# Performance work log

Measured on AMD Instinct MI355X. Metric: run time of the kernel, lower is better.

Reference implementation:

```python
import jax, jax.numpy as jnp
import numpy as np

MUL = 32            # multiplicity of each irrep (0e and 1o)
N_NODES = 50000
N_EDGES = 800000
NUM_NEIGHBORS = 16.0
SQRT3 = 3.0 ** 0.5
SILU_NORM = 1.6790  # e3nn normalize2mom constant for silu: 1/sqrt(E[silu(z)^2]), z~N(0,1)


def split_irreps(x):
    # x: [..., 128] laid out as 32x0e (32) ++ 32x1o (32*3)
    x0 = x[..., :MUL]
    x1 = x[..., MUL:].reshape(x.shape[:-1] + (MUL, 3))
    return x0, x1


def merge_irreps(x0, x1):
    return jnp.concatenate([x0, x1.reshape(x1.shape[:-2] + (MUL * 3,))], axis=-1)


def fctp_scalar(x0, x1, a, W0, W1, fan_in):
    # FullyConnectedTensorProduct(in_irreps, '1x0e', out_irreps): per-irrep linear
    # mixing scaled by scalar attr; e3nn path weight sqrt(dim_out/fan_in) times the
    # orthonormal CG (1/sqrt(dim)) folds to 1/sqrt(fan_in) for every irrep.
    s = a / jnp.sqrt(jnp.asarray(fan_in, x0.dtype))
    o0 = (x0 @ W0) * s
    o1 = jnp.einsum('nud,uw->nwd', x1, W1) * s[..., None]
    return o0, o1


def setup_inputs() -> dict:
    key = jax.random.key(0)
    ks = jax.random.split(key, 17)
    inp = dict(
        node_input=jax.random.normal(ks[0], (N_NODES, 4 * MUL), jnp.float32),
        node_attr=jnp.ones((N_NODES, 1), jnp.float32),
        edge_src=jax.random.randint(ks[1], (N_EDGES,), 0, N_NODES),
        edge_dst=jax.random.randint(ks[2], (N_EDGES,), 0, N_NODES),
        edge_attr=jax.random.normal(ks[3], (N_EDGES, 4), jnp.float32),
        edge_scalars=jax.random.normal(ks[4], (N_EDGES, 64), jnp.float32),
    )
    p = lambda k, sh: jax.random.normal(k, sh, jnp.float32)  # e3nn init: N(0,1)
    inp.update(
        W_sc0=p(ks[5], (MUL, MUL)), W_sc1=p(ks[6], (MUL, MUL)),
        W_l1_0=p(ks[7], (MUL, MUL)), W_l1_1=p(ks[8], (MUL, MUL)),
        W_fc1=p(ks[9], (64, 64)), W_fc2=p(ks[10], (64, 4 * MUL)),
        W_l2_A0=p(ks[11], (MUL, MUL)), W_l2_B0=p(ks[12], (MUL, MUL)),
        W_l2_C1=p(ks[13], (MUL, MUL)), W_l2_D1=p(ks[14], (MUL, MUL)),
        W_l3_A=p(ks[15], (MUL, 1)), W_l3_B=p(ks[16], (MUL, 1)),
    )
    return inp


def reference(node_input, node_attr, edge_src, edge_dst, edge_attr, edge_scalars,
              W_sc0, W_sc1, W_l1_0, W_l1_1, W_fc1, W_fc2,
              W_l2_A0, W_l2_B0, W_l2_C1, W_l2_D1, W_l3_A, W_l3_B):
    n = node_input.shape[0]
    x0, x1 = split_irreps(node_input)

    # per-edge TP weights from MLP on edge scalars (e3nn FullyConnectedNet)
    h = SILU_NORM * jax.nn.silu(edge_scalars @ (W_fc1 / 8.0))  # /sqrt(64)
    weight = h @ (W_fc2 / 8.0)                                  # [E, 128]

    # self connection (sc) and lin1 (FCTP with scalar node attr, fan_in = 32)
    sc0, sc1 = fctp_scalar(x0, x1, node_attr, W_sc0, W_sc1, MUL)
    f0, f1 = fctp_scalar(x0, x1, node_attr, W_l1_0, W_l1_1, MUL)

    # gather source-node features per edge
    g0 = f0[edge_src]          # [E, 32]
    g1 = f1[edge_src]          # [E, 32, 3]
    e0 = edge_attr[:, :1]      # [E, 1]  0e
    e1 = edge_attr[:, 1:]      # [E, 3]  1o

    # weight layout follows instruction order: (0e*0e->0e), (0e*1o->1o), (1o*0e->1o), (1o*1o->0e)
    wA, wC, wD, wB = (weight[:, :MUL], weight[:, MUL:2 * MUL],
                      weight[:, 2 * MUL:3 * MUL], weight[:, 3 * MUL:])
    # weighted CG tensor product ('uvu'); e3nn path weights sqrt(dim_out) folded with
    # orthonormal wigner-3j entries (1/sqrt(3) for l=1 couplings)
    outA = wA * g0 * e0                                    # [E,32]   0e x 0e -> 0e
    outB = wB * jnp.einsum('euk,ek->eu', g1, e1) / SQRT3   # [E,32]   1o x 1o -> 0e
    outC = (wC * g0)[..., None] * e1[:, None, :]           # [E,32,3] 0e x 1o -> 1o
    outD = wD[..., None] * g1 * e0[..., None]              # [E,32,3] 1o x 0e -> 1o

    # scatter-add aggregation to destination nodes
    seg = lambda v: jax.ops.segment_sum(v, edge_dst, num_segments=n)
    inv = 1.0 / jnp.sqrt(jnp.asarray(NUM_NEIGHBORS, node_input.dtype))
    mA, mB, mC, mD = seg(outA) * inv, seg(outB) * inv, seg(outC) * inv, seg(outD) * inv

    # lin2: irreps_mid (32x0e+32x0e+32x1o+32x1o) -> output, fan_in = 64 per output irrep
    s = node_attr / 8.0  # attr / sqrt(64)
    c0 = (mA @ W_l2_A0 + mB @ W_l2_B0) * s
    c1 = (jnp.einsum('nud,uw->nwd', mC, W_l2_C1)
          + jnp.einsum('nud,uw->nwd', mD, W_l2_D1)) * s[..., None]

    # lin3: irreps_mid -> 0e gate angle (only 0e chunks contribute)
    angle = 0.1 * (mA @ W_l3_A + mB @ W_l3_B) * s          # [N, 1]
    cos, sin = jnp.cos(angle), jnp.sin(angle)              # sc.output_mask is all ones

    return cos * merge_irreps(sc0, sc1) + sin * merge_irreps(c0, c1)
```

## Files before the change

kernel.cpp:

```cpp
#include <hip/hip_runtime.h>
#include <stdint.h>

#define N_NODES 50000
#define N_EDGES 800000
#define CAP 64
#define NTILES 50000
#define NSB 49

typedef _Float16 f16x8 __attribute__((ext_vector_type(8)));
typedef _Float16 f16x2 __attribute__((ext_vector_type(2)));
typedef float    f32x4 __attribute__((ext_vector_type(4)));

static __device__ __forceinline__ uint32_t pk16(float a, float b) {
    return __builtin_bit_cast(uint32_t, __builtin_amdgcn_cvt_pkrtz(a, b));
}
static __device__ __forceinline__ float lo16(uint32_t v) {
    f16x2 h = __builtin_bit_cast(f16x2, v); return (float)h[0];
}
static __device__ __forceinline__ float hi16(uint32_t v) {
    f16x2 h = __builtin_bit_cast(f16x2, v); return (float)h[1];
}

__global__ __launch_bounds__(256) void k_node_f(
        const float* __restrict__ x, const float* __restrict__ attr,
        const float* __restrict__ W0, const float* __restrict__ W1,
        uint32_t* __restrict__ fh)
{
    const int wv = threadIdx.x >> 6;
    const int t  = threadIdx.x & 63;
    const int node = blockIdx.x*4 + wv;
    if (node >= N_NODES) return;
    __shared__ float xs[4][128];
    xs[wv][t]      = x[(size_t)node*128 + t];
    xs[wv][64 + t] = x[(size_t)node*128 + 64 + t];
    float a = attr[node] * 0.17677669529663689f;
    float s0 = 0.f, s1 = 0.f;
    if (t < 32) {
        #pragma unroll
        for (int v = 0; v < 32; ++v) {
            s0 += xs[wv][v] * W0[v*32 + t];
            s1 += xs[wv][32 + v*3 + 0] * W1[v*32 + t];
        }
    } else {
        int u = t - 32;
        #pragma unroll
        for (int v = 0; v < 32; ++v) {
            s0 += xs[wv][32 + v*3 + 1] * W1[v*32 + u];
            s1 += xs[wv][32 + v*3 + 2] * W1[v*32 + u];
        }
    }
    fh[(size_t)node*64 + t] = pk16(s0*a, s1*a);
}

__global__ void k_ticket(const int* __restrict__ dst, int* __restrict__ cnt,
                         uint8_t* __restrict__ slot8) {
    int e = blockIdx.x*256 + threadIdx.x;
    if (e >= N_EDGES) return;
    int d = dst[e];
    int slot = atomicAdd(&cnt[d], 1);
    slot8[e] = (uint8_t)min(slot, 255);
}

__global__ __launch_bounds__(1024) void k_scan1(const int* __restrict__ cnt,
                                                int* __restrict__ offs,
                                                int* __restrict__ bsum) {
    __shared__ int sh[1024];
    int t = threadIdx.x, i = blockIdx.x*1024 + t;
    int v = (i < N_NODES) ? min(cnt[i], CAP) : 0;
    sh[t] = v; __syncthreads();
    #pragma unroll
    for (int off = 1; off < 1024; off <<= 1) {
        int u = (t >= off) ? sh[t - off] : 0;
        __syncthreads();
        sh[t] += u;
        __syncthreads();
    }
    if (i < N_NODES) offs[i] = sh[t] - v;
    if (t == 1023) bsum[blockIdx.x] = sh[t];
}

__global__ void k_scan2(const int* __restrict__ bsum, int* __restrict__ bbase,
                        int* __restrict__ offs) {
    int t = threadIdx.x;
    int v = (t < NSB) ? bsum[t] : 0;
    int inc = v;
    #pragma unroll
    for (int off = 1; off < 64; off <<= 1) {
        int u = __shfl_up(inc, off);
        if (t >= off) inc += u;
    }
    if (t < NSB) bbase[t] = inc - v;
    if (t == NSB - 1) offs[N_NODES] = inc;
}

__global__ __launch_bounds__(1024) void k_scan3(int* __restrict__ offs,
                                                const int* __restrict__ bbase) {
    int i = blockIdx.x*1024 + threadIdx.x;
    if (i < N_NODES) offs[i] += bbase[blockIdx.x];
}

__global__ void k_scatter(const int* __restrict__ dst, const int* __restrict__ esrc,
                          const float* __restrict__ eattr,
                          const uint8_t* __restrict__ slot8,
                          const int* __restrict__ offs,
                          int2* __restrict__ csr_se, float4* __restrict__ csr_e1) {
    int e = blockIdx.x*256 + threadIdx.x;
    if (e >= N_EDGES) return;
    int slot = slot8[e];
    if (slot >= CAP) return;
    int pos = offs[dst[e]] + slot;
    csr_se[pos] = make_int2(e, esrc[e]);
    float4 ea = *(const float4*)(eattr + (size_t)e*4);
    csr_e1[pos] = make_float4(ea.y, ea.z, ea.w, ea.x);
}

__global__ __launch_bounds__(256) void k_edge_w(
    const float* __restrict__ escal, const float* __restrict__ eattr,
    const float* __restrict__ Wfc1, const float* __restrict__ Wfc2,
    uint32_t* __restrict__ weight)
{
    __shared__ __align__(16) _Float16 lds_h[4][16][72];
    __shared__ __align__(16) uint32_t lds_o[4][16][64];

    const int wv   = threadIdx.x >> 6;
    const int lane = threadIdx.x & 63;
    const int rl   = lane & 15;
    const int g4   = lane >> 4;

    f16x8 w1f[2][4];
    #pragma unroll
    for (int ks = 0; ks < 2; ++ks)
      #pragma unroll
      for (int jt = 0; jt < 4; ++jt)
        #pragma unroll
        for (int i = 0; i < 8; ++i)
          w1f[ks][jt][i] = (_Float16)(Wfc1[(ks*32 + g4*8 + i)*64 + jt*16 + rl] * 0.125f);
    f16x8 w2f[2][8];
    #pragma unroll
    for (int ks = 0; ks < 2; ++ks)
      #pragma unroll
      for (int jt = 0; jt < 8; ++jt)
        #pragma unroll
        for (int i = 0; i < 8; ++i)
          w2f[ks][jt][i] = (_Float16)(Wfc2[(ks*32 + g4*8 + i)*128 + jt*16 + rl] * 0.125f);

    const int w  = blockIdx.x*4 + wv;
    const int t0 = w*8;
    const int t1 = (t0 + 8 < NTILES) ? t0 + 8 : NTILES;

    for (int tt = t0; tt < t1; ++tt) {
        const int eb = tt*16;
        f16x8 af[2];
        #pragma unroll
        for (int ks = 0; ks < 2; ++ks) {
            const float* p = escal + (size_t)(eb + rl)*64 + ks*32 + g4*8;
            float4 lo = *(const float4*)(p);
            float4 hi = *(const float4*)(p + 4);
            af[ks][0]=(_Float16)lo.x; af[ks][1]=(_Float16)lo.y;
            af[ks][2]=(_Float16)lo.z; af[ks][3]=(_Float16)lo.w;
            af[ks][4]=(_Float16)hi.x; af[ks][5]=(_Float16)hi.y;
            af[ks][6]=(_Float16)hi.z; af[ks][7]=(_Float16)hi.w;
        }
        float e0L = eattr[(size_t)(eb + rl)*4];

        f32x4 hacc[4];
        #pragma unroll
        for (int jt = 0; jt < 4; ++jt) {
            f32x4 z = {0.f,0.f,0.f,0.f};
            z = __builtin_amdgcn_mfma_f32_16x16x32_f16(af[0], w1f[0][jt], z, 0,0,0);
            z = __builtin_amdgcn_mfma_f32_16x16x32_f16(af[1], w1f[1][jt], z, 0,0,0);
            hacc[jt] = z;
        }
        #pragma unroll
        for (int jt = 0; jt < 4; ++jt)
          #pragma unroll
          for (int r = 0; r < 4; ++r) {
            float v = hacc[jt][r];
            float s = 1.679f * v / (1.f + __expf(-v));
            lds_h[wv][g4*4 + r][jt*16 + rl] = (_Float16)s;
          }
        f16x8 a2[2];
        #pragma unroll
        for (int ks = 0; ks < 2; ++ks)
            a2[ks] = *reinterpret_cast<const f16x8*>(&lds_h[wv][rl][ks*32 + g4*8]);

        f32x4 z[8];
        #pragma unroll
        for (int jt = 0; jt < 8; ++jt) {
            f32x4 zz = {0.f,0.f,0.f,0.f};
            zz = __builtin_amdgcn_mfma_f32_16x16x32_f16(a2[0], w2f[0][jt], zz, 0,0,0);
            zz = __builtin_amdgcn_mfma_f32_16x16x32_f16(a2[1], w2f[1][jt], zz, 0,0,0);
            z[jt] = zz;
        }

        #pragma unroll
        for (int pg = 0; pg < 2; ++pg)
          #pragma unroll
          for (int r = 0; r < 4; ++r) {
            float e0r = __shfl(e0L, g4*4 + r);
            float loA = z[pg][r]     * (0.25f * e0r);
            float hiC = z[2 + pg][r] * 0.25f;
            float loD = z[4 + pg][r] * (0.25f * e0r);
            float hiB = z[6 + pg][r] * 0.14433756729740643f;
            lds_o[wv][g4*4 + r][pg*16 + rl]      = pk16(loA, hiC);
            lds_o[wv][g4*4 + r][32 + pg*16 + rl] = pk16(loD, hiB);
          }

        uint32_t* wg = weight + (size_t)eb*64;
        const uint32_t* lo32 = &lds_o[wv][0][0];
        #pragma unroll
        for (int pq = 0; pq < 4; ++pq) {
            *(uint4*)(wg + pq*256 + lane*4) = *(const uint4*)(lo32 + pq*256 + lane*4);
        }
    }
}

__global__ __launch_bounds__(256, 6) void k_main(
    const float* __restrict__ x, const float* __restrict__ attr,
    const uint32_t* __restrict__ weight, const int2* __restrict__ csr_se,
    const float4* __restrict__ csr_e1,
    const float* __restrict__ Wsc0, const float* __restrict__ Wsc1,
    const float* __restrict__ WA0,  const float* __restrict__ WB0,
    const float* __restrict__ WC1,  const float* __restrict__ WD1,
    const float* __restrict__ W3A,  const float* __restrict__ W3B,
    const uint32_t* __restrict__ fh, const int* __restrict__ offs,
    float* __restrict__ out)
{
    __shared__ float lds_m[4][256];

    const int wv   = threadIdx.x >> 6;
    const int lane = threadIdx.x & 63;
    const int u    = lane & 31;
    const int half = lane >> 5;
    const int node = blockIdx.x*4 + wv;
    if (node >= N_NODES) return;

    const int o0  = __builtin_amdgcn_readfirstlane(offs[node]);
    const int deg = __builtin_amdgcn_readfirstlane(offs[node + 1]) - o0;

    float mAB = 0.f, mCD0 = 0.f, mCD1 = 0.f, mCD2 = 0.f;

    for (int b = 0; b < deg; b += 16) {
        int nb = min(16, deg - b);
        uint32_t wp[16], ga[16], gbv[16];
        #pragma unroll
        for (int j = 0; j < 16; ++j) if (j < nb) {
            int pos = o0 + b + j;
            int2 se = csr_se[pos];
            wp[j] = weight[(size_t)se.x*64 + lane];
            const uint32_t* fr = fh + (size_t)se.y*64;
            ga[j] = fr[u];
            if (half) gbv[j] = fr[32 + u];
        }
        #pragma unroll
        for (int j = 0; j < 16; ++j) if (j < nb) {
            int pos = o0 + b + j;
            float4 v = csr_e1[pos];
            float e1x = v.x, e1y = v.y, e1z = v.z;
            float lo = lo16(wp[j]), hi = hi16(wp[j]);
            if (half == 0) {
                float g0 = lo16(ga[j]);
                mAB += lo * g0;
                float tc = hi * g0;
                mCD0 += tc*e1x; mCD1 += tc*e1y; mCD2 += tc*e1z;
            } else {
                float gx = hi16(ga[j]);
                float gy = lo16(gbv[j]), gz = hi16(gbv[j]);
                mAB += hi * (gx*e1x + gy*e1y + gz*e1z);
                mCD0 += lo*gx; mCD1 += lo*gy; mCD2 += lo*gz;
            }
        }
    }

    float* M = lds_m[wv];
    if (half == 0) {
        M[u] = mAB;
        M[64  + u*3 + 0] = mCD0; M[64  + u*3 + 1] = mCD1; M[64  + u*3 + 2] = mCD2;
    } else {
        M[32 + u] = mAB;
        M[160 + u*3 + 0] = mCD0; M[160 + u*3 + 1] = mCD1; M[160 + u*3 + 2] = mCD2;
    }

    float a    = attr[node];
    float a8   = a * 0.125f;
    float as32 = a * 0.17677669529663689f;

    const float w3 = (half == 0) ? W3A[u] : W3B[u];
    float tpart = (half == 0) ? M[u] * w3 : M[32 + u] * w3;
    #pragma unroll
    for (int off = 32; off > 0; off >>= 1) tpart += __shfl_xor(tpart, off);
    float angle = 0.1f * tpart * a8;
    float sn, cs; __sincosf(angle, &sn, &cs);

    const float* xr = x + (size_t)node*128;
    #pragma unroll
    for (int pass = 0; pass < 2; ++pass) {
        int c = lane + pass*64;
        bool A = (c < 32);
        int cc = c - 32;
        int wq = cc / 3, d = cc - 3*wq;
        int sT = A ? 1 : 3;
        const float* pT1 = A ? &M[0]        : &M[64 + d];
        const float* pT2 = A ? &M[32]       : &M[160 + d];
        const float* pX  = A ? xr           : xr + 32 + d;
        int k = A ? c : wq;
        const float* pWa = (A ? WA0  : WC1)  + k;
        const float* pWb = (A ? WB0  : WD1)  + k;
        const float* pWx = (A ? Wsc0 : Wsc1) + k;
        float s1 = 0.f, s2 = 0.f;
        #pragma unroll
        for (int uu = 0; uu < 32; ++uu) {
            s1 += pT1[uu*sT] * pWa[uu*32] + pT2[uu*sT] * pWb[uu*32];
            s2 += pX[uu*sT]  * pWx[uu*32];
        }
        out[(size_t)node*128 + c] = cs*(s2*as32) + sn*(s1*a8);
    }
}

extern "C" void kernel_launch(void* const* d_in, const int* in_sizes, int n_in,
                              void* d_out, int out_size, void* d_ws, size_t ws_size,
                              hipStream_t stream) {
    const float* node_input = (const float*)d_in[0];
    const float* node_attr  = (const float*)d_in[1];
    const int*   edge_src   = (const int*)  d_in[2];
    const int*   edge_dst   = (const int*)  d_in[3];
    const float* edge_attr  = (const float*)d_in[4];
    const float* edge_scal  = (const float*)d_in[5];
    const float* W_sc0 = (const float*)d_in[6];
    const float* W_sc1 = (const float*)d_in[7];
    const float* W_l10 = (const float*)d_in[8];
    const float* W_l11 = (const float*)d_in[9];
    const float* W_fc1 = (const float*)d_in[10];
    const float* W_fc2 = (const float*)d_in[11];
    const float* W_A0  = (const float*)d_in[12];
    const float* W_B0  = (const float*)d_in[13];
    const float* W_C1  = (const float*)d_in[14];
    const float* W_D1  = (const float*)d_in[15];
    const float* W_3A  = (const float*)d_in[16];
    const float* W_3B  = (const float*)d_in[17];
    float* out = (float*)d_out;

    char* p = (char*)d_ws;
    auto alloc = [&](size_t bytes) { char* r = p; p += (bytes + 15) & ~(size_t)15; return r; };
    uint32_t* fh      = (uint32_t*)alloc((size_t)N_NODES*64*4);
    int*      cnt     = (int*)     alloc((size_t)N_NODES*4);
    int*      offs    = (int*)     alloc((size_t)(N_NODES+1)*4);
    uint8_t*  slot8   = (uint8_t*) alloc((size_t)N_EDGES);
    int*      bsum    = (int*)     alloc((size_t)NSB*4);
    int*      bbase   = (int*)     alloc((size_t)NSB*4);
    int2*     csr_se  = (int2*)    alloc((size_t)N_EDGES*8);
    float4*   csr_e1  = (float4*)  alloc((size_t)N_EDGES*16);
    uint32_t* weight  = (uint32_t*)alloc((size_t)N_EDGES*64*4);

    hipMemsetAsync(cnt, 0, (size_t)N_NODES*4, stream);
    k_node_f <<<(N_NODES+3)/4, 256, 0, stream>>>(node_input, node_attr, W_l10, W_l11, fh);
    k_ticket <<<(N_EDGES+255)/256, 256, 0, stream>>>(edge_dst, cnt, slot8);
    k_scan1  <<<NSB, 1024, 0, stream>>>(cnt, offs, bsum);
    k_scan2  <<<1, 64, 0, stream>>>(bsum, bbase, offs);
    k_scan3  <<<NSB, 1024, 0, stream>>>(offs, bbase);
    k_scatter<<<(N_EDGES+255)/256, 256, 0, stream>>>(edge_dst, edge_src, edge_attr,
               slot8, offs, csr_se, csr_e1);
    k_edge_w <<<1563, 256, 0, stream>>>(edge_scal, edge_attr, W_fc1, W_fc2, weight);
    k_main   <<<(N_NODES+3)/4, 256, 0, stream>>>(node_input, node_attr, weight, csr_se, csr_e1,
               W_sc0, W_sc1, W_A0, W_B0, W_C1, W_D1, W_3A, W_3B, fh, offs, out);
}
```

Before: 389.2 us.

## Move self-connection linear into node kernel and share weight loads across node pairs

Computes the self-connection (sc) linear in k_node_f and stores it as packed fp16 per node, so k_main no longer reads x or applies Wsc. The epilogue of k_main now has each thread handle one output channel for two nodes, reusing each loaded WA/WB/WC/WD weight twice. It also shrinks csr_e1 from float4 to a 12-byte struct. The costs are an extra node-sized buffer, fp16 rounding of the sc term, a block-wide __syncthreads, and removal of the early-exit node bound check, which is safe only because N_NODES is divisible by 4.

```diff
diff --git a/kernel.cpp b/kernel.cpp
--- a/kernel.cpp
+++ b/kernel.cpp
@@ -11,6 +11,8 @@
 typedef _Float16 f16x2 __attribute__((ext_vector_type(2)));
 typedef float    f32x4 __attribute__((ext_vector_type(4)));
 
+struct F3 { float x, y, z; };
+
 static __device__ __forceinline__ uint32_t pk16(float a, float b) {
     return __builtin_bit_cast(uint32_t, __builtin_amdgcn_cvt_pkrtz(a, b));
 }
@@ -24,7 +26,8 @@
 __global__ __launch_bounds__(256) void k_node_f(
         const float* __restrict__ x, const float* __restrict__ attr,
         const float* __restrict__ W0, const float* __restrict__ W1,
-        uint32_t* __restrict__ fh)
+        const float* __restrict__ Wsc0, const float* __restrict__ Wsc1,
+        uint32_t* __restrict__ fh, uint32_t* __restrict__ sch)
 {
     const int wv = threadIdx.x >> 6;
     const int t  = threadIdx.x & 63;
@@ -34,6 +37,7 @@
     xs[wv][t]      = x[(size_t)node*128 + t];
     xs[wv][64 + t] = x[(size_t)node*128 + 64 + t];
     float a = attr[node] * 0.17677669529663689f;
+
     float s0 = 0.f, s1 = 0.f;
     if (t < 32) {
         #pragma unroll
@@ -50,6 +54,23 @@
         }
     }
     fh[(size_t)node*64 + t] = pk16(s0*a, s1*a);
+
+    float c0 = 0.f, c1 = 0.f;
+    if (t < 32) {
+        #pragma unroll
+        for (int v = 0; v < 32; ++v) c0 += xs[wv][v] * Wsc0[v*32 + t];
+    } else {
+        int cc = t - 32, w = cc / 3, d = cc - 3*w;
+        #pragma unroll
+        for (int v = 0; v < 32; ++v) c0 += xs[wv][32 + v*3 + d] * Wsc1[v*32 + w];
+    }
+    {
+        int cc = t + 32;
+        int w = cc / 3, d = cc - 3*w;
+        #pragma unroll
+        for (int v = 0; v < 32; ++v) c1 += xs[wv][32 + v*3 + d] * Wsc1[v*32 + w];
+    }
+    sch[(size_t)node*64 + t] = pk16(c0*a, c1*a);
 }
 
 __global__ void k_ticket(const int* __restrict__ dst, int* __restrict__ cnt,
@@ -103,7 +124,7 @@
                           const float* __restrict__ eattr,
                           const uint8_t* __restrict__ slot8,
                           const int* __restrict__ offs,
-                          int2* __restrict__ csr_se, float4* __restrict__ csr_e1) {
+                          int2* __restrict__ csr_se, F3* __restrict__ csr_e1) {
     int e = blockIdx.x*256 + threadIdx.x;
     if (e >= N_EDGES) return;
     int slot = slot8[e];
@@ -111,7 +132,7 @@
     int pos = offs[dst[e]] + slot;
     csr_se[pos] = make_int2(e, esrc[e]);
     float4 ea = *(const float4*)(eattr + (size_t)e*4);
-    csr_e1[pos] = make_float4(ea.y, ea.z, ea.w, ea.x);
+    csr_e1[pos] = {ea.y, ea.z, ea.w};
 }
 
 __global__ __launch_bounds__(256) void k_edge_w(
@@ -216,24 +237,23 @@
 }
 
 __global__ __launch_bounds__(256, 6) void k_main(
-    const float* __restrict__ x, const float* __restrict__ attr,
+    const float* __restrict__ attr,
     const uint32_t* __restrict__ weight, const int2* __restrict__ csr_se,
-    const float4* __restrict__ csr_e1,
-    const float* __restrict__ Wsc0, const float* __restrict__ Wsc1,
+    const F3* __restrict__ csr_e1,
     const float* __restrict__ WA0,  const float* __restrict__ WB0,
     const float* __restrict__ WC1,  const float* __restrict__ WD1,
     const float* __restrict__ W3A,  const float* __restrict__ W3B,
-    const uint32_t* __restrict__ fh, const int* __restrict__ offs,
-    float* __restrict__ out)
+    const uint32_t* __restrict__ fh, const uint32_t* __restrict__ sch,
+    const int* __restrict__ offs,   float* __restrict__ out)
 {
     __shared__ float lds_m[4][256];
+    __shared__ float2 lds_p[4];
 
     const int wv   = threadIdx.x >> 6;
     const int lane = threadIdx.x & 63;
     const int u    = lane & 31;
     const int half = lane >> 5;
     const int node = blockIdx.x*4 + wv;
-    if (node >= N_NODES) return;
 
     const int o0  = __builtin_amdgcn_readfirstlane(offs[node]);
     const int deg = __builtin_amdgcn_readfirstlane(offs[node + 1]) - o0;
@@ -255,7 +275,7 @@
         #pragma unroll
         for (int j = 0; j < 16; ++j) if (j < nb) {
             int pos = o0 + b + j;
-            float4 v = csr_e1[pos];
+            F3 v = csr_e1[pos];
             float e1x = v.x, e1y = v.y, e1z = v.z;
             float lo = lo16(wp[j]), hi = hi16(wp[j]);
             if (half == 0) {
@@ -281,40 +301,45 @@
         M[160 + u*3 + 0] = mCD0; M[160 + u*3 + 1] = mCD1; M[160 + u*3 + 2] = mCD2;
     }
 
-    float a    = attr[node];
-    float a8   = a * 0.125f;
-    float as32 = a * 0.17677669529663689f;
-
+    float a  = attr[node];
+    float a8 = a * 0.125f;
     const float w3 = (half == 0) ? W3A[u] : W3B[u];
     float tpart = (half == 0) ? M[u] * w3 : M[32 + u] * w3;
     #pragma unroll
     for (int off = 32; off > 0; off >>= 1) tpart += __shfl_xor(tpart, off);
     float angle = 0.1f * tpart * a8;
     float sn, cs; __sincosf(angle, &sn, &cs);
-
-    const float* xr = x + (size_t)node*128;
-    #pragma unroll
-    for (int pass = 0; pass < 2; ++pass) {
-        int c = lane + pass*64;
-        bool A = (c < 32);
-        int cc = c - 32;
-        int wq = cc / 3, d = cc - 3*wq;
-        int sT = A ? 1 : 3;
-        const float* pT1 = A ? &M[0]        : &M[64 + d];
-        const float* pT2 = A ? &M[32]       : &M[160 + d];
-        const float* pX  = A ? xr           : xr + 32 + d;
-        int k = A ? c : wq;
-        const float* pWa = (A ? WA0  : WC1)  + k;
-        const float* pWb = (A ? WB0  : WD1)  + k;
-        const float* pWx = (A ? Wsc0 : Wsc1) + k;
-        float s1 = 0.f, s2 = 0.f;
-        #pragma unroll
-        for (int uu = 0; uu < 32; ++uu) {
-            s1 += pT1[uu*sT] * pWa[uu*32] + pT2[uu*sT] * pWb[uu*32];
-            s2 += pX[uu*sT]  * pWx[uu*32];
-        }
-        out[(size_t)node*128 + c] = cs*(s2*as32) + sn*(s1*a8);
-    }
+    if (lane == 0) lds_p[wv] = make_float2(cs, sn * a8);
+    __syncthreads();
+
+    const int t   = threadIdx.x;
+    const int c   = t & 127;
+    const int grp = t >> 7;
+    const float* M0 = lds_m[grp*2 + 0];
+    const float* M1 = lds_m[grp*2 + 1];
+    bool A = (c < 32);
+    int cc = c - 32;
+    int wq = cc / 3, d = cc - 3*wq;
+    int b1 = A ? 0  : 64 + d;
+    int b2 = A ? 32 : 160 + d;
+    int sT = A ? 1 : 3;
+    const float* pWa = (A ? WA0 : WC1) + (A ? c : wq);
+    const float* pWb = (A ? WB0 : WD1) + (A ? c : wq);
+    float sa = 0.f, sb = 0.f;
+    #pragma unroll
+    for (int uu = 0; uu < 32; ++uu) {
+        float wa = pWa[uu*32], wb = pWb[uu*32];
+        sa += M0[b1 + uu*sT] * wa + M0[b2 + uu*sT] * wb;
+        sb += M1[b1 + uu*sT] * wa + M1[b2 + uu*sT] * wb;
+    }
+    int n0 = blockIdx.x*4 + grp*2;
+    float2 p0 = lds_p[grp*2 + 0], p1 = lds_p[grp*2 + 1];
+    uint32_t sp0 = sch[(size_t)n0*64 + (c & 63)];
+    uint32_t sp1 = sch[(size_t)(n0 + 1)*64 + (c & 63)];
+    float sc0 = (c < 64) ? lo16(sp0) : hi16(sp0);
+    float sc1 = (c < 64) ? lo16(sp1) : hi16(sp1);
+    out[(size_t)n0*128 + c]       = p0.x*sc0 + p0.y*sa;
+    out[(size_t)(n0 + 1)*128 + c] = p1.x*sc1 + p1.y*sb;
 }
 
 extern "C" void kernel_launch(void* const* d_in, const int* in_sizes, int n_in,
@@ -349,11 +374,13 @@
     int*      bsum    = (int*)     alloc((size_t)NSB*4);
     int*      bbase   = (int*)     alloc((size_t)NSB*4);
     int2*     csr_se  = (int2*)    alloc((size_t)N_EDGES*8);
-    float4*   csr_e1  = (float4*)  alloc((size_t)N_EDGES*16);
+    F3*       csr_e1  = (F3*)      alloc((size_t)N_EDGES*12);
     uint32_t* weight  = (uint32_t*)alloc((size_t)N_EDGES*64*4);
+    uint32_t* sch     = (uint32_t*)alloc((size_t)N_NODES*64*4);
 
     hipMemsetAsync(cnt, 0, (size_t)N_NODES*4, stream);
-    k_node_f <<<(N_NODES+3)/4, 256, 0, stream>>>(node_input, node_attr, W_l10, W_l11, fh);
+    k_node_f <<<(N_NODES+3)/4, 256, 0, stream>>>(node_input, node_attr, W_l10, W_l11,
+               W_sc0, W_sc1, fh, sch);
     k_ticket <<<(N_EDGES+255)/256, 256, 0, stream>>>(edge_dst, cnt, slot8);
     k_scan1  <<<NSB, 1024, 0, stream>>>(cnt, offs, bsum);
     k_scan2  <<<1, 64, 0, stream>>>(bsum, bbase, offs);
@@ -361,6 +388,6 @@
     k_scatter<<<(N_EDGES+255)/256, 256, 0, stream>>>(edge_dst, edge_src, edge_attr,
                slot8, offs, csr_se, csr_e1);
     k_edge_w <<<1563, 256, 0, stream>>>(edge_scal, edge_attr, W_fc1, W_fc2, weight);
-    k_main   <<<(N_NODES+3)/4, 256, 0, stream>>>(node_input, node_attr, weight, csr_se, csr_e1,
-               W_sc0, W_sc1, W_A0, W_B0, W_C1, W_D1, W_3A, W_3B, fh, offs, out);
-}
+    k_main   <<<(N_NODES+3)/4, 256, 0, stream>>>(node_attr, weight, csr_se, csr_e1,
+               W_A0, W_B0, W_C1, W_D1, W_3A, W_3B, fh, sch, offs, out);
+}
```

Result: no change. 386.8 us (-0.6%).
